# Kernel optimization log

Measured on AMD Instinct MI355X. Metric: run time of the kernel, lower is better.

The kernel has to match this reference:

```python
import jax, jax.numpy as jnp
import numpy as np

N = 100000   # nodes
E = 1600000  # edges (before self-loops)
H = 4        # heads
C = 16       # out channels per head
NEG_SLOPE = 0.2


def _gat_layer(x, src, dst, W, a_src, a_dst, b):
    # x: [N, Fin]; W: [Fin, H*C]; a_src/a_dst: [H, C]; b: [H*C]
    h = (x @ W).reshape(N, H, C)                       # [N, H, C]
    e_s = jnp.einsum('nhc,hc->nh', h, a_src)           # [N, H]
    e_d = jnp.einsum('nhc,hc->nh', h, a_dst)           # [N, H]
    e = e_s[src] + e_d[dst]                            # [E', H]
    e = jax.nn.leaky_relu(e, NEG_SLOPE)
    # segment softmax over destination nodes
    m = jax.ops.segment_max(e, dst, num_segments=N)    # [N, H]
    ex = jnp.exp(e - m[dst])
    s = jax.ops.segment_sum(ex, dst, num_segments=N)   # [N, H]
    alpha = ex / (s[dst] + 1e-16)                      # [E', H]
    msg = alpha[:, :, None] * h[src]                   # [E', H, C]
    out = jax.ops.segment_sum(msg, dst, num_segments=N)  # [N, H, C]
    return out.reshape(N, H * C) + b


def setup_inputs() -> dict:
    key = jax.random.key(0)
    ks = jax.random.split(key, 24)
    g = lambda k, shp, sc=0.1: (jax.random.normal(k, shp, jnp.float32) * sc)
    inp = {
        'x': jax.random.normal(ks[0], (N, 1), jnp.float32),
        'edge_index': jax.random.randint(ks[1], (2, E), 0, N, dtype=jnp.int32),
        # GAT layer 0: in=1
        'W0': g(ks[2], (1, H * C)), 'as0': g(ks[3], (H, C)), 'ad0': g(ks[4], (H, C)), 'b0': jnp.zeros((H * C,), jnp.float32),
        # GAT layer 1: in=64
        'W1': g(ks[5], (H * C, H * C)), 'as1': g(ks[6], (H, C)), 'ad1': g(ks[7], (H, C)), 'b1': jnp.zeros((H * C,), jnp.float32),
        # GAT layer 2: in=64
        'W2': g(ks[8], (H * C, H * C)), 'as2': g(ks[9], (H, C)), 'ad2': g(ks[10], (H, C)), 'b2': jnp.zeros((H * C,), jnp.float32),
        # latent MLP: Linear(64,64) -> ReLU -> Linear(64,16)
        'lw1': g(ks[11], (H * C, 64)), 'lb1': jnp.zeros((64,), jnp.float32),
        'lw2': g(ks[12], (64, 16)), 'lb2': jnp.zeros((16,), jnp.float32),
        # decoder: Linear(16,4) -> Softmax
        'dw': g(ks[13], (16, 4)), 'db': jnp.zeros((4,), jnp.float32),
    }
    return inp


def reference(x, edge_index, W0, as0, ad0, b0, W1, as1, ad1, b1, W2, as2, ad2, b2, lw1, lb1, lw2, lb2, dw, db):
    # add self-loops (PyG GATConv default add_self_loops=True)
    loops = jnp.arange(N, dtype=edge_index.dtype)
    src = jnp.concatenate([edge_index[0], loops])
    dst = jnp.concatenate([edge_index[1], loops])
    h = _gat_layer(x, src, dst, W0, as0, ad0, b0)
    h = _gat_layer(h, src, dst, W1, as1, ad1, b1)
    h = _gat_layer(h, src, dst, W2, as2, ad2, b2)
    h = jax.nn.relu(h @ lw1 + lb1)
    h = h @ lw2 + lb2
    logits = h @ dw + db
    return jax.nn.softmax(logits, axis=-1)
```

## Files before the change

### kernel.cpp

```cpp
#include <hip/hip_runtime.h>
#include <hip/hip_fp16.h>
#include <math.h>

#define NN 100000
#define EE 1600000
#define EP (EE + NN)
#define NEG 0.2f
#define TN 128
#define BW 256
#define NB 391
#define CHUNK 4096
#define SSTRIDE 5120
#define SCAP 5120
#define SPLIT 50000

typedef __attribute__((ext_vector_type(2))) float floatx2;

__device__ inline unsigned pk_fp8x4(float a, float b, float c, float d) {
    unsigned r = __builtin_amdgcn_cvt_pk_fp8_f32(a, b, 0u, false);
    r = __builtin_amdgcn_cvt_pk_fp8_f32(c, d, r, true);
    return r;
}

__device__ __forceinline__ void accum_fp8p(uint2 raw, float p, floatx2* acc) {
    floatx2 p2; p2[0] = p; p2[1] = p;
    acc[0] += p2 * __builtin_amdgcn_cvt_pk_f32_fp8(raw.x, false);
    acc[1] += p2 * __builtin_amdgcn_cvt_pk_f32_fp8(raw.x, true);
    acc[2] += p2 * __builtin_amdgcn_cvt_pk_f32_fp8(raw.y, false);
    acc[3] += p2 * __builtin_amdgcn_cvt_pk_f32_fp8(raw.y, true);
}


__global__ __launch_bounds__(512) void partition_k(const int* __restrict__ ei, int* __restrict__ gcur,
                                                   unsigned int* __restrict__ arena) {
    __shared__ int lh[512], lsc[512], lcur[512];
    __shared__ unsigned int staged[CHUNK];
    __shared__ unsigned short stb[CHUNK];
    int tid = threadIdx.x;
    int c0 = blockIdx.x * CHUNK;
    int csize = min(CHUNK, EP - c0);
    lh[tid] = 0;
    __syncthreads();
    unsigned int myv[8];
    int myb[8];
#pragma unroll
    for (int i = 0; i < 8; i++) {
        int e = c0 + i * 512 + tid;
        if (e < c0 + csize) {
            int d = (e < EE) ? ei[EE + e] : (e - EE);
            int sv = (e < EE) ? ei[e] : d;
            int b = d >> 8;
            myv[i] = ((unsigned)(d - (b << 8)) << 17) | (unsigned)sv;
            myb[i] = b;
            atomicAdd(&lh[b], 1);
        } else myb[i] = -1;
    }
    __syncthreads();
    int v = lh[tid];
    lsc[tid] = v;
    __syncthreads();
    for (int o = 1; o < 512; o <<= 1) {
        int t = (tid >= o) ? lsc[tid - o] : 0;
        __syncthreads();
        lsc[tid] += t;
        __syncthreads();
    }
    lcur[tid] = lsc[tid] - v;
    __syncthreads();
#pragma unroll
    for (int i = 0; i < 8; i++) {
        if (myb[i] >= 0) {
            int idx = atomicAdd(&lcur[myb[i]], 1);
            staged[idx] = myv[i];
            stb[idx] = (unsigned short)myb[i];
        }
    }
    __syncthreads();
    if (tid < NB && lh[tid] > 0) {
        int base = atomicAdd(&gcur[tid], lh[tid]);
        lsc[tid] = tid * SSTRIDE + base - (lcur[tid] - lh[tid]);
    }
    __syncthreads();
    for (int i = tid; i < csize; i += 512) {
        unsigned int val = staged[i];
        arena[lsc[stb[i]] + i] = val;
    }
}

__global__ __launch_bounds__(512) void bscan_k(const int* __restrict__ gcur, int* __restrict__ bbase,
                                               int* __restrict__ rowptr) {
    __shared__ int s[512];
    int tid = threadIdx.x;
    int v = (tid < NB) ? gcur[tid] : 0;
    s[tid] = v;
    __syncthreads();
    for (int o = 1; o < 512; o <<= 1) {
        int t = (tid >= o) ? s[tid - o] : 0;
        __syncthreads();
        s[tid] += t;
        __syncthreads();
    }
    int excl = s[tid] - v;
    if (tid <= NB) bbase[tid] = excl;
    if (tid == 0) rowptr[NN] = EP;
}

__global__ __launch_bounds__(512) void csr_scatter_k(const int* __restrict__ bbase, const int* __restrict__ gcur,
                                                     const unsigned int* __restrict__ arena,
                                                     int* __restrict__ rowptr, int* __restrict__ rowmid,
                                                     int* __restrict__ edge_src) {
    __shared__ int cnt[512], sc[512];
    __shared__ unsigned int stg[SCAP];
    int tid = threadIdx.x;
    int b = blockIdx.x;
    int e0 = bbase[b];
    int sz = gcur[b];
    int abase = b * SSTRIDE;
    cnt[tid] = 0;
    __syncthreads();
    for (int i = tid; i < sz; i += 512) {
        unsigned int v = arena[abase + i];
        if (i < SCAP) stg[i] = v;
        int dl = v >> 17;
        int hb = ((v & 0x1FFFFu) >= (unsigned)SPLIT) ? 1 : 0;
        atomicAdd(&cnt[(dl << 1) | hb], 1);
    }
    __syncthreads();
    int v = cnt[tid];
    sc[tid] = v;
    __syncthreads();
    for (int o = 1; o < 512; o <<= 1) {
        int t = (tid >= o) ? sc[tid - o] : 0;
        __syncthreads();
        sc[tid] += t;
        __syncthreads();
    }
    int excl = sc[tid] - v;
    int dl = tid >> 1, hb = tid & 1;
    int d = (b << 8) + dl;
    if (d < NN) {
        if (hb == 0) rowptr[d] = e0 + excl;
        else         rowmid[d] = e0 + excl;
    }
    sc[tid] = excl;
    __syncthreads();
    for (int i = tid; i < sz; i += 512) {
        unsigned int val = (i < SCAP) ? stg[i] : arena[abase + i];
        int dli = val >> 17;
        unsigned srcv = val & 0x1FFFFu;
        int hbi = (srcv >= (unsigned)SPLIT) ? 1 : 0;
        int p = atomicAdd(&sc[(dli << 1) | hbi], 1);
        edge_src[e0 + p] = (int)srcv;
    }
}


__global__ __launch_bounds__(256) void gather0_k(const float* __restrict__ x, const float* __restrict__ W0,
                                                 const float* __restrict__ as_, const float* __restrict__ ad_,
                                                 const int* __restrict__ rowptr, const int* __restrict__ edge_src,
                                                 const float* __restrict__ b, __half* __restrict__ hout) {
    __shared__ float W0l[64], asl[64], adl[64], bl[64];
    int tid = threadIdx.x;
    if (tid < 64) { W0l[tid] = W0[tid]; asl[tid] = as_[tid]; adl[tid] = ad_[tid]; bl[tid] = b[tid]; }
    __syncthreads();
    int wv = (blockIdx.x * 256 + tid) >> 6;
    int lane = tid & 63;
    if (wv >= NN) return;
    int q = lane >> 2, head = lane & 3;
    float cs = 0.f, cd = 0.f;
#pragma unroll
    for (int c = 0; c < 16; c++) {
        float w = W0l[head * 16 + c];
        cs += w * asl[head * 16 + c];
        cd += w * adl[head * 16 + c];
    }
    int beg = rowptr[wv], end = rowptr[wv + 1];
    float xd = x[wv];
    float num = 0.f, den = 0.f;
    for (int e0 = beg; e0 < end; e0 += 16) {
        int e = e0 + q;
        bool vld = e < end;
        int ee = vld ? e : (end - 1);
        int src = edge_src[ee];
        float xs = x[src];
        float ev = xs * cs + xd * cd;
        ev = ev > 0.f ? ev : NEG * ev;
        float p = vld ? __expf(ev) : 0.f;
        num += p * xs;
        den += p;
    }
    num += __shfl_xor(num, 4);  num += __shfl_xor(num, 8);
    num += __shfl_xor(num, 16); num += __shfl_xor(num, 32);
    den += __shfl_xor(den, 4);  den += __shfl_xor(den, 8);
    den += __shfl_xor(den, 16); den += __shfl_xor(den, 32);
    float nh = __shfl(num, lane >> 4);
    float dh = __shfl(den, lane >> 4);
    float val = nh / (dh + 1e-16f);
    float hv = val * W0l[lane] + bl[lane];
    hout[((size_t)wv << 6) + lane] = __float2half(hv);
}


__global__ __launch_bounds__(256) void transform64_k(const __half* __restrict__ hin, const float* __restrict__ W,
                                                     const float* __restrict__ as_, const float* __restrict__ ad_,
                                                     unsigned char* __restrict__ h8, float* __restrict__ es, float* __restrict__ ed) {
    __shared__ float At[64 * TN];
    __shared__ float Wl[64 * 64];
    int tid = threadIdx.x;
    for (int i = tid; i < 4096; i += 256) Wl[i] = W[i];
    int n0 = blockIdx.x * TN;
    {
        int row = tid >> 1, hf = tid & 1;
        int n = n0 + row;
        const uint4* src = (const uint4*)(hin + ((size_t)n << 6) + (hf << 5));
#pragma unroll
        for (int i = 0; i < 4; i++) {
            uint4 raw = make_uint4(0, 0, 0, 0);
            if (n < NN) raw = src[i];
            __half2* hh = (__half2*)&raw;
            int c = (hf << 5) + (i << 3);
#pragma unroll
            for (int j = 0; j < 4; j++) {
                float2 f = __half22float2(hh[j]);
                At[(c + 2 * j) * TN + row]     = f.x;
                At[(c + 2 * j + 1) * TN + row] = f.y;
            }
        }
    }
    __syncthreads();
    int c = tid & 15, r = tid >> 4;
    float acc[8][4];
#pragma unroll
    for (int i = 0; i < 8; i++)
#pragma unroll
        for (int j = 0; j < 4; j++) acc[i][j] = 0.f;
#pragma unroll 4
    for (int k = 0; k < 64; k++) {
        float4 a0 = *(float4*)&At[k * TN + r * 8];
        float4 a1 = *(float4*)&At[k * TN + r * 8 + 4];
        float4 w  = *(float4*)&Wl[k * 64 + c * 4];
        float av[8] = {a0.x, a0.y, a0.z, a0.w, a1.x, a1.y, a1.z, a1.w};
#pragma unroll
        for (int i = 0; i < 8; i++) {
            acc[i][0] += av[i] * w.x; acc[i][1] += av[i] * w.y;
            acc[i][2] += av[i] * w.z; acc[i][3] += av[i] * w.w;
        }
    }
    int head = c >> 2, qq = c & 3;
    float as0v = as_[head * 16 + qq * 4], as1v = as_[head * 16 + qq * 4 + 1];
    float as2v = as_[head * 16 + qq * 4 + 2], as3v = as_[head * 16 + qq * 4 + 3];
    float ad0v = ad_[head * 16 + qq * 4], ad1v = ad_[head * 16 + qq * 4 + 1];
    float ad2v = ad_[head * 16 + qq * 4 + 2], ad3v = ad_[head * 16 + qq * 4 + 3];
#pragma unroll
    for (int i = 0; i < 8; i++) {
        int n = n0 + r * 8 + i;
        float pes = acc[i][0] * as0v + acc[i][1] * as1v + acc[i][2] * as2v + acc[i][3] * as3v;
        float ped = acc[i][0] * ad0v + acc[i][1] * ad1v + acc[i][2] * ad2v + acc[i][3] * ad3v;
        pes += __shfl_xor(pes, 1); pes += __shfl_xor(pes, 2);
        ped += __shfl_xor(ped, 1); ped += __shfl_xor(ped, 2);
        if (n < NN) {
            unsigned rq = pk_fp8x4(acc[i][0], acc[i][1], acc[i][2], acc[i][3]);
            *(unsigned*)(h8 + ((size_t)n << 6) + (c << 2)) = rq;
            if (qq == 0) { es[n * 4 + head] = pes; ed[n * 4 + head] = ped; }
        }
    }
}


__device__ __forceinline__ void gspan2(const unsigned char* __restrict__ h8j, const float* __restrict__ es,
                                       const int* __restrict__ edge_src,
                                       int lo0, int hi0, int lo1, int hi1, int q, int head,
                                       float edvA, float edvB, floatx2* accA, floatx2* accB,
                                       float& sA, float& sB) {
    int iters = max((hi0 - lo0 + 7) >> 3, (hi1 - lo1 + 7) >> 3);
    int cl0 = min(lo0, EP - 1), cl1 = min(lo1, EP - 1);
    int k = 0;
    for (; k + 2 <= iters; k += 2) {
        int eA0 = lo0 + (k << 3) + q, eA1 = eA0 + 8;
        int eB0 = lo1 + (k << 3) + q, eB1 = eB0 + 8;
        bool vA0 = eA0 < hi0, vA1 = eA1 < hi0;
        bool vB0 = eB0 < hi1, vB1 = eB1 < hi1;
        int srcA0 = edge_src[vA0 ? eA0 : cl0];
        int srcA1 = edge_src[vA1 ? eA1 : cl0];
        int srcB0 = edge_src[vB0 ? eB0 : cl1];
        int srcB1 = edge_src[vB1 ? eB1 : cl1];
        uint2 rawA0 = *(const uint2*)(h8j + ((size_t)srcA0 << 6));
        uint2 rawA1 = *(const uint2*)(h8j + ((size_t)srcA1 << 6));
        uint2 rawB0 = *(const uint2*)(h8j + ((size_t)srcB0 << 6));
        uint2 rawB1 = *(const uint2*)(h8j + ((size_t)srcB1 << 6));
        float esvA0 = es[srcA0 * 4 + head];
        float esvA1 = es[srcA1 * 4 + head];
        float esvB0 = es[srcB0 * 4 + head];
        float esvB1 = es[srcB1 * 4 + head];
        float evA0 = esvA0 + edvA; evA0 = evA0 > 0.f ? evA0 : NEG * evA0;
        float evA1 = esvA1 + edvA; evA1 = evA1 > 0.f ? evA1 : NEG * evA1;
        float evB0 = esvB0 + edvB; evB0 = evB0 > 0.f ? evB0 : NEG * evB0;
        float evB1 = esvB1 + edvB; evB1 = evB1 > 0.f ? evB1 : NEG * evB1;
        float pA0 = vA0 ? __expf(evA0) : 0.f;
        float pA1 = vA1 ? __expf(evA1) : 0.f;
        float pB0 = vB0 ? __expf(evB0) : 0.f;
        float pB1 = vB1 ? __expf(evB1) : 0.f;
        accum_fp8p(rawA0, pA0, accA);
        accum_fp8p(rawA1, pA1, accA);
        accum_fp8p(rawB0, pB0, accB);
        accum_fp8p(rawB1, pB1, accB);
        sA += pA0 + pA1;
        sB += pB0 + pB1;
    }
    if (k < iters) {
        int eA = lo0 + (k << 3) + q;
        int eB = lo1 + (k << 3) + q;
        bool vA = eA < hi0;
        bool vB = eB < hi1;
        int srcA = edge_src[vA ? eA : cl0];
        int srcB = edge_src[vB ? eB : cl1];
        uint2 rawA = *(const uint2*)(h8j + ((size_t)srcA << 6));
        uint2 rawB = *(const uint2*)(h8j + ((size_t)srcB << 6));
        float esvA = es[srcA * 4 + head];
        float esvB = es[srcB * 4 + head];
        float evA = esvA + edvA; evA = evA > 0.f ? evA : NEG * evA;
        float evB = esvB + edvB; evB = evB > 0.f ? evB : NEG * evB;
        float pA = vA ? __expf(evA) : 0.f;
        float pB = vB ? __expf(evB) : 0.f;
        accum_fp8p(rawA, pA, accA);
        accum_fp8p(rawB, pB, accB);
        sA += pA;
        sB += pB;
    }
}

__global__ __launch_bounds__(256) void gather_k(const unsigned char* __restrict__ h8, const float* __restrict__ es,
                                                const float* __restrict__ ed, const int* __restrict__ rowptr,
                                                const int* __restrict__ rowmid, const int* __restrict__ edge_src,
                                                const float* __restrict__ b, __half* __restrict__ hout) {
    int pr = (blockIdx.x * 256 + threadIdx.x) >> 6;
    int lane = threadIdx.x & 63;
    int nA = pr * 2;
    if (nA >= NN) return;
    int nB = nA + 1;
    bool hasB = nB < NN;
    int q = lane >> 3, j = lane & 7, head = j >> 1;
    const unsigned char* h8j = h8 + (j << 3);
    int begA = rowptr[nA], midA = rowmid[nA], endA = rowptr[nA + 1];
    int begB = hasB ? rowptr[nB] : begA;
    int midB = hasB ? rowmid[nB] : begA;
    int endB = hasB ? rowptr[nB + 1] : begA;
    float edvA = ed[nA * 4 + head];
    float edvB = hasB ? ed[nB * 4 + head] : 0.f;
    floatx2 accA[4], accB[4];
#pragma unroll
    for (int t = 0; t < 4; t++) { accA[t] = (floatx2)(0.f); accB[t] = (floatx2)(0.f); }
    float sA = 0.f, sB = 0.f;
    gspan2(h8j, es, edge_src, begA, midA, begB, midB, q, head, edvA, edvB, accA, accB, sA, sB);
    gspan2(h8j, es, edge_src, midA, endA, midB, endB, q, head, edvA, edvB, accA, accB, sA, sB);
    float fA[8], fB[8];
#pragma unroll
    for (int t = 0; t < 4; t++) {
        fA[2 * t] = accA[t][0]; fA[2 * t + 1] = accA[t][1];
        fB[2 * t] = accB[t][0]; fB[2 * t + 1] = accB[t][1];
    }
#pragma unroll
    for (int t = 0; t < 8; t++) {
        fA[t] += __shfl_xor(fA[t], 8);
        fA[t] += __shfl_xor(fA[t], 16);
        fA[t] += __shfl_xor(fA[t], 32);
        fB[t] += __shfl_xor(fB[t], 8);
        fB[t] += __shfl_xor(fB[t], 16);
        fB[t] += __shfl_xor(fB[t], 32);
    }
    sA += __shfl_xor(sA, 8); sA += __shfl_xor(sA, 16); sA += __shfl_xor(sA, 32);
    sB += __shfl_xor(sB, 8); sB += __shfl_xor(sB, 16); sB += __shfl_xor(sB, 32);
    if (q == 0) {
        const float4* bp = (const float4*)(b + j * 8);
        float4 b0 = bp[0], b1 = bp[1];
        {
            float inv = 1.0f / (sA + 1e-16f);
            union { __half2 h2[4]; uint4 u; } pk;
            pk.h2[0] = __floats2half2_rn(fA[0] * inv + b0.x, fA[1] * inv + b0.y);
            pk.h2[1] = __floats2half2_rn(fA[2] * inv + b0.z, fA[3] * inv + b0.w);
            pk.h2[2] = __floats2half2_rn(fA[4] * inv + b1.x, fA[5] * inv + b1.y);
            pk.h2[3] = __floats2half2_rn(fA[6] * inv + b1.z, fA[7] * inv + b1.w);
            *(uint4*)(hout + ((size_t)nA << 6) + (j << 3)) = pk.u;
        }
        if (hasB) {
            float inv = 1.0f / (sB + 1e-16f);
            union { __half2 h2[4]; uint4 u; } pk;
            pk.h2[0] = __floats2half2_rn(fB[0] * inv + b0.x, fB[1] * inv + b0.y);
            pk.h2[1] = __floats2half2_rn(fB[2] * inv + b0.z, fB[3] * inv + b0.w);
            pk.h2[2] = __floats2half2_rn(fB[4] * inv + b1.x, fB[5] * inv + b1.y);
            pk.h2[3] = __floats2half2_rn(fB[6] * inv + b1.z, fB[7] * inv + b1.w);
            *(uint4*)(hout + ((size_t)nB << 6) + (j << 3)) = pk.u;
        }
    }
}


__global__ __launch_bounds__(256) void mlp_k(const __half* __restrict__ h, const float* __restrict__ lw1,
                                             const float* __restrict__ lb1, const float* __restrict__ lw2,
                                             const float* __restrict__ lb2, const float* __restrict__ dw,
                                             const float* __restrict__ db, float* __restrict__ out) {
    __shared__ float At[64 * TN];
    __shared__ float W1l[4096];
    __shared__ float W2l[1024];
    __shared__ float dwl[64];
    __shared__ float dbl[4];
    int tid = threadIdx.x;
    for (int i = tid; i < 4096; i += 256) W1l[i] = lw1[i];
    for (int i = tid; i < 1024; i += 256) W2l[i] = lw2[i];
    if (tid < 64) dwl[tid] = dw[tid];
    if (tid < 4) dbl[tid] = db[tid];
    int n0 = blockIdx.x * TN;
    {
        int row = tid >> 1, hf = tid & 1;
        int n = n0 + row;
        const uint4* src = (const uint4*)(h + ((size_t)n << 6) + (hf << 5));
#pragma unroll
        for (int i = 0; i < 4; i++) {
            uint4 raw = make_uint4(0, 0, 0, 0);
            if (n < NN) raw = src[i];
            __half2* hh = (__half2*)&raw;
            int c = (hf << 5) + (i << 3);
#pragma unroll
            for (int j = 0; j < 4; j++) {
                float2 f = __half22float2(hh[j]);
                At[(c + 2 * j) * TN + row]     = f.x;
                At[(c + 2 * j + 1) * TN + row] = f.y;
            }
        }
    }
    __syncthreads();
    int c = tid & 15, r = tid >> 4;
    float acc[8][4];
#pragma unroll
    for (int i = 0; i < 8; i++)
#pragma unroll
        for (int j = 0; j < 4; j++) acc[i][j] = 0.f;
#pragma unroll 4
    for (int k = 0; k < 64; k++) {
        float4 a0 = *(float4*)&At[k * TN + r * 8];
        float4 a1 = *(float4*)&At[k * TN + r * 8 + 4];
        float4 w  = *(float4*)&W1l[k * 64 + c * 4];
        float av[8] = {a0.x, a0.y, a0.z, a0.w, a1.x, a1.y, a1.z, a1.w};
#pragma unroll
        for (int i = 0; i < 8; i++) {
            acc[i][0] += av[i] * w.x; acc[i][1] += av[i] * w.y;
            acc[i][2] += av[i] * w.z; acc[i][3] += av[i] * w.w;
        }
    }
    float b1v0 = lb1[c * 4], b1v1 = lb1[c * 4 + 1], b1v2 = lb1[c * 4 + 2], b1v3 = lb1[c * 4 + 3];
    __syncthreads();
#pragma unroll
    for (int i = 0; i < 8; i++) {
        int n = r * 8 + i;
        At[(c * 4 + 0) * TN + n] = fmaxf(acc[i][0] + b1v0, 0.f);
        At[(c * 4 + 1) * TN + n] = fmaxf(acc[i][1] + b1v1, 0.f);
        At[(c * 4 + 2) * TN + n] = fmaxf(acc[i][2] + b1v2, 0.f);
        At[(c * 4 + 3) * TN + n] = fmaxf(acc[i][3] + b1v3, 0.f);
    }
    __syncthreads();
    float acc2[8];
#pragma unroll
    for (int i = 0; i < 8; i++) acc2[i] = 0.f;
#pragma unroll 4
    for (int k = 0; k < 64; k++) {
        float4 a0 = *(float4*)&At[k * TN + r * 8];
        float4 a1 = *(float4*)&At[k * TN + r * 8 + 4];
        float wv = W2l[k * 16 + c];
        acc2[0] += a0.x * wv; acc2[1] += a0.y * wv; acc2[2] += a0.z * wv; acc2[3] += a0.w * wv;
        acc2[4] += a1.x * wv; acc2[5] += a1.y * wv; acc2[6] += a1.z * wv; acc2[7] += a1.w * wv;
    }
    float b2v = lb2[c];
#pragma unroll
    for (int i = 0; i < 8; i++) W1l[c * TN + r * 8 + i] = acc2[i] + b2v;
    __syncthreads();
    if (tid < TN) {
        int n = n0 + tid;
        if (n < NN) {
            float lg0 = dbl[0], lg1 = dbl[1], lg2 = dbl[2], lg3 = dbl[3];
#pragma unroll
            for (int k = 0; k < 16; k++) {
                float a = W1l[k * TN + tid];
                lg0 += a * dwl[k * 4];     lg1 += a * dwl[k * 4 + 1];
                lg2 += a * dwl[k * 4 + 2]; lg3 += a * dwl[k * 4 + 3];
            }
            float mx = fmaxf(fmaxf(lg0, lg1), fmaxf(lg2, lg3));
            float e0 = __expf(lg0 - mx), e1 = __expf(lg1 - mx), e2 = __expf(lg2 - mx), e3 = __expf(lg3 - mx);
            float inv = 1.0f / (e0 + e1 + e2 + e3);
            *(float4*)(out + (size_t)n * 4) = make_float4(e0 * inv, e1 * inv, e2 * inv, e3 * inv);
        }
    }
}


extern "C" void kernel_launch(void* const* d_in, const int* in_sizes, int n_in,
                              void* d_out, int out_size, void* d_ws, size_t ws_size,
                              hipStream_t stream) {
    const float* x   = (const float*)d_in[0];
    const int*   ei  = (const int*)d_in[1];
    const float* W0  = (const float*)d_in[2];
    const float* as0 = (const float*)d_in[3];
    const float* ad0 = (const float*)d_in[4];
    const float* b0  = (const float*)d_in[5];
    const float* W1  = (const float*)d_in[6];
    const float* as1 = (const float*)d_in[7];
    const float* ad1 = (const float*)d_in[8];
    const float* b1  = (const float*)d_in[9];
    const float* W2  = (const float*)d_in[10];
    const float* as2 = (const float*)d_in[11];
    const float* ad2 = (const float*)d_in[12];
    const float* b2  = (const float*)d_in[13];
    const float* lw1 = (const float*)d_in[14];
    const float* lb1 = (const float*)d_in[15];
    const float* lw2 = (const float*)d_in[16];
    const float* lb2 = (const float*)d_in[17];
    const float* dw  = (const float*)d_in[18];
    const float* db  = (const float*)d_in[19];
    float* out = (float*)d_out;

    char* p = (char*)d_ws;
    size_t off = 0;
    auto alloc = [&](size_t n) -> void* {
        void* r = p + off;
        off = (off + n + 255) & ~(size_t)255;
        return r;
    };
    __half* hB     = (__half*)alloc((size_t)NN * 64 * 2);
    __half* hC     = (__half*)alloc((size_t)NN * 64 * 2);
    unsigned char* h8 = (unsigned char*)alloc((size_t)NN * 64);
    float*  es     = (float*)alloc((size_t)NN * 4 * 4);
    float*  ed     = (float*)alloc((size_t)NN * 4 * 4);
    int*    rowptr = (int*)alloc((size_t)(NN + 1) * 4);
    int*    rowmid = (int*)alloc((size_t)NN * 4);
    int*    edge_src = (int*)alloc((size_t)EP * 4);
    unsigned int* arena = (unsigned int*)alloc((size_t)NB * SSTRIDE * 4);
    int*    gcur   = (int*)alloc(512 * 4);
    int*    bbase  = (int*)alloc(513 * 4);

    hipMemsetAsync(gcur, 0, 512 * 4, stream);

    partition_k<<<(EP + CHUNK - 1) / CHUNK, 512, 0, stream>>>(ei, gcur, arena);
    bscan_k<<<1, 512, 0, stream>>>(gcur, bbase, rowptr);
    csr_scatter_k<<<NB, 512, 0, stream>>>(bbase, gcur, arena, rowptr, rowmid, edge_src);

    int nb_tile = (NN + TN - 1) / TN;
    int nb_wave = (NN + 3) / 4;
    int nb_pair = ((NN + 1) / 2 + 3) / 4;

    gather0_k<<<nb_wave, 256, 0, stream>>>(x, W0, as0, ad0, rowptr, edge_src, b0, hB);

    transform64_k<<<nb_tile, 256, 0, stream>>>(hB, W1, as1, ad1, h8, es, ed);
    gather_k<<<nb_pair, 256, 0, stream>>>(h8, es, ed, rowptr, rowmid, edge_src, b1, hC);

    transform64_k<<<nb_tile, 256, 0, stream>>>(hC, W2, as2, ad2, h8, es, ed);
    gather_k<<<nb_pair, 256, 0, stream>>>(h8, es, ed, rowptr, rowmid, edge_src, b2, hB);

    mlp_k<<<nb_tile, 256, 0, stream>>>(hB, lw1, lb1, lw2, lb2, dw, db, out);
}
```

Baseline: 313.3 us.

## Drop source-half CSR split, use wave-shuffle scans, simplify gather loop

Removes the per-destination split of edges by source index half (rowmid), so the CSR build only buckets by destination and the gather kernel walks one span per node instead of two. The block-wide Hillis-Steele scans in partition and csr_scatter are replaced with wave-level shuffle scans plus a small cross-wave fixup, cutting many barriers. The gather loop is no longer unrolled by two. The trade-off is losing whatever cache locality the source-half ordering gave to h8 gathers and the extra memory-level parallelism of the unrolled loop.

```diff
diff --git a/kernel.cpp b/kernel.cpp
--- a/kernel.cpp
+++ b/kernel.cpp
@@ -12,7 +12,6 @@
 #define CHUNK 4096
 #define SSTRIDE 5120
 #define SCAP 5120
-#define SPLIT 50000
 
 typedef __attribute__((ext_vector_type(2))) float floatx2;
 
@@ -30,13 +29,24 @@
     acc[3] += p2 * __builtin_amdgcn_cvt_pk_f32_fp8(raw.y, true);
 }
 
+__device__ __forceinline__ int wave_iscan(int v, int lane) {
+#pragma unroll
+    for (int o = 1; o < 64; o <<= 1) {
+        int t = __shfl_up(v, o);
+        if (lane >= o) v += t;
+    }
+    return v;
+}
+
 
 __global__ __launch_bounds__(512) void partition_k(const int* __restrict__ ei, int* __restrict__ gcur,
                                                    unsigned int* __restrict__ arena) {
-    __shared__ int lh[512], lsc[512], lcur[512];
+    __shared__ int lh[512], lcur[512], lbase[512];
+    __shared__ int wsum[8];
     __shared__ unsigned int staged[CHUNK];
     __shared__ unsigned short stb[CHUNK];
     int tid = threadIdx.x;
+    int lane = tid & 63, wid = tid >> 6;
     int c0 = blockIdx.x * CHUNK;
     int csize = min(CHUNK, EP - c0);
     lh[tid] = 0;
@@ -57,15 +67,17 @@
     }
     __syncthreads();
     int v = lh[tid];
-    lsc[tid] = v;
-    __syncthreads();
-    for (int o = 1; o < 512; o <<= 1) {
-        int t = (tid >= o) ? lsc[tid - o] : 0;
-        __syncthreads();
-        lsc[tid] += t;
-        __syncthreads();
-    }
-    lcur[tid] = lsc[tid] - v;
+    int isc = wave_iscan(v, lane);
+    if (lane == 63) wsum[wid] = isc;
+    __syncthreads();
+    if (tid == 0) {
+        int run = 0;
+#pragma unroll
+        for (int w = 0; w < 8; w++) { int t = wsum[w]; wsum[w] = run; run += t; }
+    }
+    __syncthreads();
+    int excl = isc - v + wsum[wid];
+    lcur[tid] = excl;
     __syncthreads();
 #pragma unroll
     for (int i = 0; i < 8; i++) {
@@ -76,14 +88,14 @@
         }
     }
     __syncthreads();
-    if (tid < NB && lh[tid] > 0) {
-        int base = atomicAdd(&gcur[tid], lh[tid]);
-        lsc[tid] = tid * SSTRIDE + base - (lcur[tid] - lh[tid]);
+    if (tid < NB && v > 0) {
+        int base = atomicAdd(&gcur[tid], v);
+        lbase[tid] = tid * SSTRIDE + base - excl;
     }
     __syncthreads();
     for (int i = tid; i < csize; i += 512) {
         unsigned int val = staged[i];
-        arena[lsc[stb[i]] + i] = val;
+        arena[lbase[stb[i]] + i] = val;
     }
 }
 
@@ -107,50 +119,49 @@
 
 __global__ __launch_bounds__(512) void csr_scatter_k(const int* __restrict__ bbase, const int* __restrict__ gcur,
                                                      const unsigned int* __restrict__ arena,
-                                                     int* __restrict__ rowptr, int* __restrict__ rowmid,
-                                                     int* __restrict__ edge_src) {
-    __shared__ int cnt[512], sc[512];
+                                                     int* __restrict__ rowptr, int* __restrict__ edge_src) {
+    __shared__ int cnt[256], sc[256];
+    __shared__ int wsum[4];
     __shared__ unsigned int stg[SCAP];
     int tid = threadIdx.x;
     int b = blockIdx.x;
     int e0 = bbase[b];
     int sz = gcur[b];
     int abase = b * SSTRIDE;
-    cnt[tid] = 0;
+    if (tid < 256) cnt[tid] = 0;
     __syncthreads();
     for (int i = tid; i < sz; i += 512) {
         unsigned int v = arena[abase + i];
         if (i < SCAP) stg[i] = v;
-        int dl = v >> 17;
-        int hb = ((v & 0x1FFFFu) >= (unsigned)SPLIT) ? 1 : 0;
-        atomicAdd(&cnt[(dl << 1) | hb], 1);
-    }
-    __syncthreads();
-    int v = cnt[tid];
-    sc[tid] = v;
-    __syncthreads();
-    for (int o = 1; o < 512; o <<= 1) {
-        int t = (tid >= o) ? sc[tid - o] : 0;
+        atomicAdd(&cnt[v >> 17], 1);
+    }
+    __syncthreads();
+    if (tid < 256) {
+        int lane = tid & 63, wid = tid >> 6;
+        int v = cnt[tid];
+        int isc = wave_iscan(v, lane);
+        if (lane == 63) wsum[wid] = isc;
         __syncthreads();
-        sc[tid] += t;
+        if (tid == 0) {
+            int run = 0;
+#pragma unroll
+            for (int w = 0; w < 4; w++) { int t = wsum[w]; wsum[w] = run; run += t; }
+        }
         __syncthreads();
-    }
-    int excl = sc[tid] - v;
-    int dl = tid >> 1, hb = tid & 1;
-    int d = (b << 8) + dl;
-    if (d < NN) {
-        if (hb == 0) rowptr[d] = e0 + excl;
-        else         rowmid[d] = e0 + excl;
-    }
-    sc[tid] = excl;
+        int excl = isc - v + wsum[wid];
+        int d = (b << 8) + tid;
+        if (d < NN) rowptr[d] = e0 + excl;
+        sc[tid] = excl;
+    } else {
+        __syncthreads();
+        __syncthreads();
+    }
     __syncthreads();
     for (int i = tid; i < sz; i += 512) {
         unsigned int val = (i < SCAP) ? stg[i] : arena[abase + i];
-        int dli = val >> 17;
-        unsigned srcv = val & 0x1FFFFu;
-        int hbi = (srcv >= (unsigned)SPLIT) ? 1 : 0;
-        int p = atomicAdd(&sc[(dli << 1) | hbi], 1);
-        edge_src[e0 + p] = (int)srcv;
+        int dl = val >> 17;
+        int p = atomicAdd(&sc[dl], 1);
+        edge_src[e0 + p] = (int)(val & 0x1FFFFu);
     }
 }
 
@@ -267,56 +278,37 @@
 }
 
 
-__device__ __forceinline__ void gspan2(const unsigned char* __restrict__ h8j, const float* __restrict__ es,
-                                       const int* __restrict__ edge_src,
-                                       int lo0, int hi0, int lo1, int hi1, int q, int head,
-                                       float edvA, float edvB, floatx2* accA, floatx2* accB,
-                                       float& sA, float& sB) {
-    int iters = max((hi0 - lo0 + 7) >> 3, (hi1 - lo1 + 7) >> 3);
-    int cl0 = min(lo0, EP - 1), cl1 = min(lo1, EP - 1);
-    int k = 0;
-    for (; k + 2 <= iters; k += 2) {
-        int eA0 = lo0 + (k << 3) + q, eA1 = eA0 + 8;
-        int eB0 = lo1 + (k << 3) + q, eB1 = eB0 + 8;
-        bool vA0 = eA0 < hi0, vA1 = eA1 < hi0;
-        bool vB0 = eB0 < hi1, vB1 = eB1 < hi1;
-        int srcA0 = edge_src[vA0 ? eA0 : cl0];
-        int srcA1 = edge_src[vA1 ? eA1 : cl0];
-        int srcB0 = edge_src[vB0 ? eB0 : cl1];
-        int srcB1 = edge_src[vB1 ? eB1 : cl1];
-        uint2 rawA0 = *(const uint2*)(h8j + ((size_t)srcA0 << 6));
-        uint2 rawA1 = *(const uint2*)(h8j + ((size_t)srcA1 << 6));
-        uint2 rawB0 = *(const uint2*)(h8j + ((size_t)srcB0 << 6));
-        uint2 rawB1 = *(const uint2*)(h8j + ((size_t)srcB1 << 6));
-        float esvA0 = es[srcA0 * 4 + head];
-        float esvA1 = es[srcA1 * 4 + head];
-        float esvB0 = es[srcB0 * 4 + head];
-        float esvB1 = es[srcB1 * 4 + head];
-        float evA0 = esvA0 + edvA; evA0 = evA0 > 0.f ? evA0 : NEG * evA0;
-        float evA1 = esvA1 + edvA; evA1 = evA1 > 0.f ? evA1 : NEG * evA1;
-        float evB0 = esvB0 + edvB; evB0 = evB0 > 0.f ? evB0 : NEG * evB0;
-        float evB1 = esvB1 + edvB; evB1 = evB1 > 0.f ? evB1 : NEG * evB1;
-        float pA0 = vA0 ? __expf(evA0) : 0.f;
-        float pA1 = vA1 ? __expf(evA1) : 0.f;
-        float pB0 = vB0 ? __expf(evB0) : 0.f;
-        float pB1 = vB1 ? __expf(evB1) : 0.f;
-        accum_fp8p(rawA0, pA0, accA);
-        accum_fp8p(rawA1, pA1, accA);
-        accum_fp8p(rawB0, pB0, accB);
-        accum_fp8p(rawB1, pB1, accB);
-        sA += pA0 + pA1;
-        sB += pB0 + pB1;
-    }
-    if (k < iters) {
-        int eA = lo0 + (k << 3) + q;
-        int eB = lo1 + (k << 3) + q;
-        bool vA = eA < hi0;
-        bool vB = eB < hi1;
-        int srcA = edge_src[vA ? eA : cl0];
-        int srcB = edge_src[vB ? eB : cl1];
-        uint2 rawA = *(const uint2*)(h8j + ((size_t)srcA << 6));
-        uint2 rawB = *(const uint2*)(h8j + ((size_t)srcB << 6));
+__global__ __launch_bounds__(256) void gather_k(const unsigned char* __restrict__ h8, const float* __restrict__ es,
+                                                const float* __restrict__ ed, const int* __restrict__ rowptr,
+                                                const int* __restrict__ edge_src, const float* __restrict__ b,
+                                                __half* __restrict__ hout) {
+    int pr = (blockIdx.x * 256 + threadIdx.x) >> 6;
+    int lane = threadIdx.x & 63;
+    int nA = pr * 2;
+    if (nA >= NN) return;
+    int nB = nA + 1;
+    bool hasB = nB < NN;
+    int q = lane >> 3, j = lane & 7, head = j >> 1;
+    const unsigned char* h8j = h8 + (j << 3);
+    int begA = rowptr[nA], endA = rowptr[nA + 1];
+    int begB = hasB ? rowptr[nB] : begA, endB = hasB ? rowptr[nB + 1] : begA;
+    float edvA = ed[nA * 4 + head];
+    float edvB = hasB ? ed[nB * 4 + head] : 0.f;
+    floatx2 accA[4], accB[4];
+#pragma unroll
+    for (int t = 0; t < 4; t++) { accA[t] = (floatx2)(0.f); accB[t] = (floatx2)(0.f); }
+    float sA = 0.f, sB = 0.f;
+    int iters = max((endA - begA + 7) >> 3, (endB - begB + 7) >> 3);
+    for (int k = 0; k < iters; k++) {
+        int eA = begA + (k << 3) + q;
+        int eB = begB + (k << 3) + q;
+        bool vA = eA < endA;
+        bool vB = eB < endB;
+        int srcA = edge_src[vA ? eA : begA];
+        int srcB = edge_src[vB ? eB : begB];
+        uint2 rawA = *(const uint2*)(h8j + ((unsigned)srcA << 6));
         float esvA = es[srcA * 4 + head];
+        uint2 rawB = *(const uint2*)(h8j + ((unsigned)srcB << 6));
         float esvB = es[srcB * 4 + head];
         float evA = esvA + edvA; evA = evA > 0.f ? evA : NEG * evA;
         float evB = esvB + edvB; evB = evB > 0.f ? evB : NEG * evB;
@@ -327,32 +319,6 @@
         sA += pA;
         sB += pB;
     }
-}
-
-__global__ __launch_bounds__(256) void gather_k(const unsigned char* __restrict__ h8, const float* __restrict__ es,
-                                                const float* __restrict__ ed, const int* __restrict__ rowptr,
-                                                const int* __restrict__ rowmid, const int* __restrict__ edge_src,
-                                                const float* __restrict__ b, __half* __restrict__ hout) {
-    int pr = (blockIdx.x * 256 + threadIdx.x) >> 6;
-    int lane = threadIdx.x & 63;
-    int nA = pr * 2;
-    if (nA >= NN) return;
-    int nB = nA + 1;
-    bool hasB = nB < NN;
-    int q = lane >> 3, j = lane & 7, head = j >> 1;
-    const unsigned char* h8j = h8 + (j << 3);
-    int begA = rowptr[nA], midA = rowmid[nA], endA = rowptr[nA + 1];
-    int begB = hasB ? rowptr[nB] : begA;
-    int midB = hasB ? rowmid[nB] : begA;
-    int endB = hasB ? rowptr[nB + 1] : begA;
-    float edvA = ed[nA * 4 + head];
-    float edvB = hasB ? ed[nB * 4 + head] : 0.f;
-    floatx2 accA[4], accB[4];
-#pragma unroll
-    for (int t = 0; t < 4; t++) { accA[t] = (floatx2)(0.f); accB[t] = (floatx2)(0.f); }
-    float sA = 0.f, sB = 0.f;
-    gspan2(h8j, es, edge_src, begA, midA, begB, midB, q, head, edvA, edvB, accA, accB, sA, sB);
-    gspan2(h8j, es, edge_src, midA, endA, midB, endB, q, head, edvA, edvB, accA, accB, sA, sB);
     float fA[8], fB[8];
 #pragma unroll
     for (int t = 0; t < 4; t++) {
@@ -530,7 +496,6 @@
     float*  es     = (float*)alloc((size_t)NN * 4 * 4);
     float*  ed     = (float*)alloc((size_t)NN * 4 * 4);
     int*    rowptr = (int*)alloc((size_t)(NN + 1) * 4);
-    int*    rowmid = (int*)alloc((size_t)NN * 4);
     int*    edge_src = (int*)alloc((size_t)EP * 4);
     unsigned int* arena = (unsigned int*)alloc((size_t)NB * SSTRIDE * 4);
     int*    gcur   = (int*)alloc(512 * 4);
@@ -540,7 +505,7 @@
 
     partition_k<<<(EP + CHUNK - 1) / CHUNK, 512, 0, stream>>>(ei, gcur, arena);
     bscan_k<<<1, 512, 0, stream>>>(gcur, bbase, rowptr);
-    csr_scatter_k<<<NB, 512, 0, stream>>>(bbase, gcur, arena, rowptr, rowmid, edge_src);
+    csr_scatter_k<<<NB, 512, 0, stream>>>(bbase, gcur, arena, rowptr, edge_src);
 
     int nb_tile = (NN + TN - 1) / TN;
     int nb_wave = (NN + 3) / 4;
@@ -549,10 +514,10 @@
     gather0_k<<<nb_wave, 256, 0, stream>>>(x, W0, as0, ad0, rowptr, edge_src, b0, hB);
 
     transform64_k<<<nb_tile, 256, 0, stream>>>(hB, W1, as1, ad1, h8, es, ed);
-    gather_k<<<nb_pair, 256, 0, stream>>>(h8, es, ed, rowptr, rowmid, edge_src, b1, hC);
+    gather_k<<<nb_pair, 256, 0, stream>>>(h8, es, ed, rowptr, edge_src, b1, hC);
 
     transform64_k<<<nb_tile, 256, 0, stream>>>(hC, W2, as2, ad2, h8, es, ed);
-    gather_k<<<nb_pair, 256, 0, stream>>>(h8, es, ed, rowptr, rowmid, edge_src, b2, hB);
+    gather_k<<<nb_pair, 256, 0, stream>>>(h8, es, ed, rowptr, edge_src, b2, hB);
 
     mlp_k<<<nb_tile, 256, 0, stream>>>(hB, lw1, lb1, lw2, lb2, dw, db, out);
 }
```

Result: no change. 309.8 us (median of 2 runs) (-1.1%).
